# Optimization experiments

Hardware: AMD Instinct MI355X
Metric: run time of the kernel (lower is better)

The kernel has to match this reference:

```python
import jax, jax.numpy as jnp
import numpy as np

B, S, H, D_IN, DEPTH, NPHN = 128, 1024, 256, 84, 2, 40
N_HEADS = 9  # phn, word1-3, utt1-5
EPS = 1e-5


def setup_inputs() -> dict:
    key = jax.random.key(0)
    ks = jax.random.split(key, 12)
    sc = 0.02
    x = jax.random.normal(ks[0], (B, S, D_IN), jnp.float32)
    # contiguous valid prefix then -1 padding (matches get_last_valid's assumption)
    lengths = jax.random.randint(ks[1], (B,), 1, S + 1)
    phn_vals = jax.random.randint(ks[2], (B, S), 0, NPHN - 1)
    phn = jnp.where(jnp.arange(S)[None, :] < lengths[:, None], phn_vals, -1)
    return {
        "x": x,
        "phn": phn,
        "in_proj_w": jax.random.normal(ks[3], (H, D_IN), jnp.float32) * sc,
        "in_proj_b": jnp.zeros((H,), jnp.float32),
        "phn_proj_w": jax.random.normal(ks[4], (H, NPHN), jnp.float32) * sc,
        "phn_proj_b": jnp.zeros((H,), jnp.float32),
        "w_ih": jax.random.normal(ks[5], (DEPTH, 4 * H, H), jnp.float32) * sc,
        "w_hh": jax.random.normal(ks[6], (DEPTH, 4 * H, H), jnp.float32) * sc,
        "b_ih": jnp.zeros((DEPTH, 4 * H), jnp.float32),
        "b_hh": jnp.zeros((DEPTH, 4 * H), jnp.float32),
        "ln_g": jnp.ones((N_HEADS, H), jnp.float32),
        "ln_b": jnp.zeros((N_HEADS, H), jnp.float32),
        "head_w": jax.random.normal(ks[7], (N_HEADS, H), jnp.float32) * sc,
        "head_b": jnp.zeros((N_HEADS,), jnp.float32),
    }


def _lstm(h0, w_ih, w_hh, b_ih, b_hh):
    # h0: [B,S,H]; torch gate order i,f,g,o
    seq = jnp.transpose(h0, (1, 0, 2))  # [S,B,H]
    b = h0.shape[0]
    for layer in range(DEPTH):
        Wih, Whh = w_ih[layer], w_hh[layer]
        bias = b_ih[layer] + b_hh[layer]

        def step(carry, xt, Wih=Wih, Whh=Whh, bias=bias):
            hp, cp = carry
            g = xt @ Wih.T + hp @ Whh.T + bias
            i, f, gg, o = jnp.split(g, 4, axis=-1)
            c = jax.nn.sigmoid(f) * cp + jax.nn.sigmoid(i) * jnp.tanh(gg)
            hn = jax.nn.sigmoid(o) * jnp.tanh(c)
            return (hn, c), hn

        init = (jnp.zeros((b, H), h0.dtype), jnp.zeros((b, H), h0.dtype))
        _, seq = jax.lax.scan(step, init, seq)
    return jnp.transpose(seq, (1, 0, 2))  # [B,S,H]


def reference(x, phn, in_proj_w, in_proj_b, phn_proj_w, phn_proj_b,
              w_ih, w_hh, b_ih, b_hh, ln_g, ln_b, head_w, head_b):
    b, s = x.shape[0], x.shape[1]
    mask = phn >= 0  # [B,S]
    phn_oh = jax.nn.one_hot(phn + 1, NPHN, dtype=x.dtype)
    h = (x @ in_proj_w.T + in_proj_b) + (phn_oh @ phn_proj_w.T + phn_proj_b)
    hidden = _lstm(h, w_ih, w_hh, b_ih, b_hh)  # [B,S,H]

    # All 9 heads share the LN-normalized activations; fold gamma/beta into the
    # per-head linear: score_k = <xhat, gamma_k*w_k> + <beta_k, w_k> + b_k
    mu = hidden.mean(-1, keepdims=True)
    var = ((hidden - mu) ** 2).mean(-1, keepdims=True)
    xhat = (hidden - mu) * jax.lax.rsqrt(var + EPS)
    scores = (jnp.einsum('bsh,kh->bsk', xhat, ln_g * head_w)
              + (ln_b * head_w).sum(-1) + head_b)  # [B,S,9]

    # last valid token per sequence: index before first mask==0 (or S-1 if all valid)
    first_inv = jnp.argmax(~mask, axis=1)
    idx = jnp.where(mask.all(axis=1), s - 1, first_inv - 1)  # [B]
    last = scores[jnp.arange(b), idx]  # [B,9]

    p = scores[..., 0:1]
    w1, w2, w3 = scores[..., 1:2], scores[..., 2:3], scores[..., 3:4]
    u1, u2, u3, u4, u5 = (last[:, 4 + k][:, None] for k in range(5))
    return (u1, u2, u3, u4, u5, p, w1, w2, w3)
```

## Files before the change

kernel.cpp:

```cpp
#include <hip/hip_runtime.h>


typedef _Float16 h2    __attribute__((ext_vector_type(2)));
typedef _Float16 f16x8 __attribute__((ext_vector_type(8)));
typedef float    f32x4 __attribute__((ext_vector_type(4)));

#define NW_MAT 262144

static __device__ __forceinline__ float fdot2u(unsigned int w, unsigned int h, float c){
#if defined(__has_builtin) && __has_builtin(__builtin_amdgcn_fdot2)
  return __builtin_amdgcn_fdot2(__builtin_bit_cast(h2, w), __builtin_bit_cast(h2, h), c, false);
#else
  h2 a = __builtin_bit_cast(h2, w), b = __builtin_bit_cast(h2, h);
  return c + (float)a[0]*(float)b[0] + (float)a[1]*(float)b[1];
#endif
}
static __device__ __forceinline__ float sigmf(float x){ return 1.f/(1.f + __expf(-x)); }
static __device__ __forceinline__ float tanhf_(float x){ return 1.f - 2.f/(__expf(2.f*x) + 1.f); }

__global__ void k_prep(const float* __restrict__ w_ih, const float* __restrict__ w_hh,
                       const float* __restrict__ b_ih, const float* __restrict__ b_hh,
                       const float* __restrict__ ln_g, const float* __restrict__ ln_b,
                       const float* __restrict__ head_w, const float* __restrict__ head_b,
                       _Float16* wih0, _Float16* whh0, _Float16* wih1, _Float16* whh1,
                       float* bias0, float* bias1, float* vk, float* ck)
{
  int i = blockIdx.x*256 + threadIdx.x;
  if (i < NW_MAT){
    wih0[i] = (_Float16)w_ih[i];
    whh0[i] = (_Float16)w_hh[i];
    wih1[i] = (_Float16)w_ih[NW_MAT + i];
    whh1[i] = (_Float16)w_hh[NW_MAT + i];
  }
  if (i < 1024){
    bias0[i] = b_ih[i]        + b_hh[i];
    bias1[i] = b_ih[1024 + i] + b_hh[1024 + i];
  }
  if (i < 2304) vk[i] = ln_g[i]*head_w[i];
  if (i < 9){
    float s = 0.f;
    for (int h = 0; h < 256; ++h) s += ln_b[i*256 + h]*head_w[i*256 + h];
    ck[i] = s + head_b[i];
  }
}

__global__ void k_idx(const int* __restrict__ phn, int* __restrict__ idx)
{
  int b = blockIdx.x, l = threadIdx.x;
  int found = -1;
  for (int t0 = 0; t0 < 1024; t0 += 64){
    int v = phn[b*1024 + t0 + l];
    unsigned long long m = __ballot(v < 0);
    if (m){ found = t0 + (__ffsll(m) - 1); break; }
  }
  if (l == 0) idx[b] = (found < 0) ? 1023 : found - 1;
}

__global__ void k_embed(const float* __restrict__ x, const int* __restrict__ phn,
                        const float* __restrict__ ipw, const float* __restrict__ ipb,
                        const float* __restrict__ ppw, const float* __restrict__ ppb,
                        _Float16* __restrict__ E, int Tc, int LT, int tc0)
{
  __shared__ float xs[8][84];
  __shared__ int pv[8];
  int tid = threadIdx.x;
  int m0 = blockIdx.x * 8;
  for (int i = tid; i < 8*84; i += 256){
    int r = i/84, k = i - r*84;
    int m = m0 + r; int b = m >> LT; int t = tc0 + (m & (Tc-1));
    xs[r][k] = x[((size_t)b*1024 + t)*84 + k];
  }
  if (tid < 8){
    int m = m0 + tid; int b = m >> LT; int t = tc0 + (m & (Tc-1));
    pv[tid] = phn[b*1024 + t];
  }
  __syncthreads();
  float acc[8] = {0.f,0.f,0.f,0.f,0.f,0.f,0.f,0.f};
  const float* wrow = ipw + tid*84;
  for (int k = 0; k < 84; ++k){
    float wv = wrow[k];
    #pragma unroll
    for (int r = 0; r < 8; ++r) acc[r] += wv * xs[r][k];
  }
  float base = ipb[tid] + ppb[tid];
  #pragma unroll
  for (int r = 0; r < 8; ++r){
    float e = acc[r] + base + ppw[tid*40 + (pv[r] + 1)];
    E[(size_t)(m0 + r)*256 + tid] = (_Float16)e;
  }
}

__global__ __launch_bounds__(256) void k_gemm(const _Float16* __restrict__ A,
                                              const _Float16* __restrict__ Bw,
                                              const float* __restrict__ bias,
                                              _Float16* __restrict__ C)
{
  __shared__ __align__(16) _Float16 lA[128*64];
  __shared__ __align__(16) _Float16 lB[128*64];
  int tid = threadIdx.x;
  int tm = blockIdx.x, tn = blockIdx.y;
  int l = tid & 63, w = tid >> 6;
  int wm = w >> 1, wn = w & 1;
  f32x4 acc[4][4];
  #pragma unroll
  for (int mi = 0; mi < 4; ++mi)
    #pragma unroll
    for (int ni = 0; ni < 4; ++ni) acc[mi][ni] = (f32x4){0.f,0.f,0.f,0.f};
  int rr = tid >> 3, cc = tid & 7;
  #pragma unroll 1
  for (int kb = 0; kb < 4; ++kb){
    uint4 av[4], bv[4];
    #pragma unroll
    for (int i = 0; i < 4; ++i){
      int r = rr + 32*i;
      av[i] = *(const uint4*)(A  + ((size_t)(tm*128 + r))*256 + kb*64 + cc*8);
      bv[i] = *(const uint4*)(Bw + ((size_t)(tn*128 + r))*256 + kb*64 + cc*8);
    }
    __syncthreads();
    #pragma unroll
    for (int i = 0; i < 4; ++i){
      int r = rr + 32*i;
      *(uint4*)&lA[r*64 + cc*8] = av[i];
      *(uint4*)&lB[r*64 + cc*8] = bv[i];
    }
    __syncthreads();
    #pragma unroll
    for (int kk = 0; kk < 2; ++kk){
      f16x8 aF[4], bF[4];
      #pragma unroll
      for (int mi = 0; mi < 4; ++mi)
        aF[mi] = *(const f16x8*)&lA[(wm*64 + mi*16 + (l&15))*64 + kk*32 + (l>>4)*8];
      #pragma unroll
      for (int ni = 0; ni < 4; ++ni)
        bF[ni] = *(const f16x8*)&lB[(wn*64 + ni*16 + (l&15))*64 + kk*32 + (l>>4)*8];
      #pragma unroll
      for (int mi = 0; mi < 4; ++mi)
        #pragma unroll
        for (int ni = 0; ni < 4; ++ni)
          acc[mi][ni] = __builtin_amdgcn_mfma_f32_16x16x32_f16(aF[mi], bF[ni], acc[mi][ni], 0, 0, 0);
    }
  }
  #pragma unroll
  for (int mi = 0; mi < 4; ++mi){
    #pragma unroll
    for (int ni = 0; ni < 4; ++ni){
      int n = tn*128 + wn*64 + ni*16 + (l & 15);
      float bn = bias[n];
      #pragma unroll
      for (int j = 0; j < 4; ++j){
        int m = tm*128 + wm*64 + mi*16 + (l>>4)*4 + j;
        C[(size_t)m*1024 + n] = (_Float16)(acc[mi][ni][j] + bn);
      }
    }
  }
}

__global__ __launch_bounds__(512, 2) void k_lstm(const _Float16* __restrict__ G,
                                                 const _Float16* __restrict__ W,
                                                 _Float16* __restrict__ Hout,
                                                 float* __restrict__ h_state,
                                                 float* __restrict__ c_state,
                                                 int Tc, int first)
{
  __shared__ __align__(16) unsigned int h_pk_s[128];
  __shared__ float gf[1024];
  __shared__ __align__(16) unsigned int wlds[32768];
  int tid = threadIdx.x;
  int b = blockIdx.x;
  int r0 = 2*tid, r1 = r0 + 1;
  const uint4* w0s = (const uint4*)(W + (size_t)r0*256);
  const uint4* w1s = (const uint4*)(W + (size_t)r1*256);
  uint4 w0v[24], w1v[24];
  #pragma unroll
  for (int c2 = 0; c2 < 24; ++c2){ w0v[c2] = w0s[c2]; w1v[c2] = w1s[c2]; }
  #pragma unroll
  for (int c2 = 0; c2 < 24; ++c2){
    asm volatile("" : "+v"(w0v[c2].x), "+v"(w0v[c2].y), "+v"(w0v[c2].z), "+v"(w0v[c2].w),
                      "+v"(w1v[c2].x), "+v"(w1v[c2].y), "+v"(w1v[c2].z), "+v"(w1v[c2].w));
  }
  unsigned int swz = (unsigned int)(tid & 7);
  #pragma unroll
  for (int c2 = 0; c2 < 8; ++c2){
    *(uint4*)&wlds[tid*64      + (((unsigned)c2 ^ swz)*4)] = w0s[24 + c2];
    *(uint4*)&wlds[tid*64 + 32 + (((unsigned)c2 ^ swz)*4)] = w1s[24 + c2];
  }
  float c_reg = 0.f, hn = 0.f;
  if (tid < 256){
    float hv = 0.f;
    if (!first){ hv = h_state[b*256 + tid]; c_reg = c_state[b*256 + tid]; }
    ((_Float16*)h_pk_s)[tid] = (_Float16)hv;
    hn = hv;
  }
  __syncthreads();
  const unsigned int* gbase = (const unsigned int*)G + (size_t)b*Tc*512 + tid;
  _Float16* hout = Hout + (size_t)b*Tc*256;
  unsigned int gc = gbase[0];
  for (int tl = 0; tl < Tc; ++tl){
    unsigned int gn = (tl + 1 < Tc) ? gbase[(size_t)(tl + 1)*512] : 0u;
    const uint4* hp = (const uint4*)h_pk_s;
    float acc0 = 0.f, acc1 = 0.f;
    #pragma unroll
    for (int c2 = 0; c2 < 24; ++c2){
      uint4 h4 = hp[c2];
      acc0 = fdot2u(w0v[c2].x, h4.x, acc0);
      acc0 = fdot2u(w0v[c2].y, h4.y, acc0);
      acc0 = fdot2u(w0v[c2].z, h4.z, acc0);
      acc0 = fdot2u(w0v[c2].w, h4.w, acc0);
      acc1 = fdot2u(w1v[c2].x, h4.x, acc1);
      acc1 = fdot2u(w1v[c2].y, h4.y, acc1);
      acc1 = fdot2u(w1v[c2].z, h4.z, acc1);
      acc1 = fdot2u(w1v[c2].w, h4.w, acc1);
    }
    #pragma unroll
    for (int c2 = 0; c2 < 8; ++c2){
      uint4 wv0 = *(const uint4*)&wlds[tid*64      + (((unsigned)c2 ^ swz)*4)];
      uint4 wv1 = *(const uint4*)&wlds[tid*64 + 32 + (((unsigned)c2 ^ swz)*4)];
      uint4 h4 = hp[24 + c2];
      acc0 = fdot2u(wv0.x, h4.x, acc0);
      acc0 = fdot2u(wv0.y, h4.y, acc0);
      acc0 = fdot2u(wv0.z, h4.z, acc0);
      acc0 = fdot2u(wv0.w, h4.w, acc0);
      acc1 = fdot2u(wv1.x, h4.x, acc1);
      acc1 = fdot2u(wv1.y, h4.y, acc1);
      acc1 = fdot2u(wv1.z, h4.z, acc1);
      acc1 = fdot2u(wv1.w, h4.w, acc1);
    }
    h2 gp = __builtin_bit_cast(h2, gc);
    *(float2*)&gf[r0] = make_float2(acc0 + (float)gp[0], acc1 + (float)gp[1]);
    __syncthreads();
    if (tid < 256){
      float gi = gf[tid], gfr = gf[tid + 256], gg = gf[tid + 512], go = gf[tid + 768];
      float ct = sigmf(gfr)*c_reg + sigmf(gi)*tanhf_(gg);
      c_reg = ct;
      hn = sigmf(go)*tanhf_(ct);
      ((_Float16*)h_pk_s)[tid] = (_Float16)hn;
      hout[(size_t)tl*256 + tid] = (_Float16)hn;
    }
    __syncthreads();
    gc = gn;
  }
  if (tid < 256){ h_state[b*256 + tid] = hn; c_state[b*256 + tid] = c_reg; }
}

__global__ void k_ln(const _Float16* __restrict__ H1, const float* __restrict__ vk,
                     const float* __restrict__ ck, const int* __restrict__ idx,
                     float* __restrict__ out, int Tc, int LT, int tc0)
{
  __shared__ __align__(16) float vks[9*256];
  __shared__ float cks[9];
  int tid = threadIdx.x;
  for (int i = tid; i < 2304; i += 256) vks[i] = vk[i];
  if (tid < 9) cks[tid] = ck[tid];
  __syncthreads();
  int l = tid & 63, wv = tid >> 6;
  int m = blockIdx.x*4 + wv;
  int b = m >> LT; int t = tc0 + (m & (Tc-1));
  uint2 hv = *(const uint2*)(H1 + (size_t)m*256 + l*4);
  h2 pa = __builtin_bit_cast(h2, hv.x), pb = __builtin_bit_cast(h2, hv.y);
  float f0 = pa[0], f1 = pa[1], f2 = pb[0], f3 = pb[1];
  float s = f0 + f1 + f2 + f3;
  float q = f0*f0 + f1*f1 + f2*f2 + f3*f3;
  #pragma unroll
  for (int o = 32; o > 0; o >>= 1){ s += __shfl_xor(s, o, 64); q += __shfl_xor(q, o, 64); }
  float mu = s*(1.f/256.f);
  float var = q*(1.f/256.f) - mu*mu;
  float rstd = rsqrtf(var + 1e-5f);
  float xh0 = (f0 - mu)*rstd, xh1 = (f1 - mu)*rstd, xh2 = (f2 - mu)*rstd, xh3 = (f3 - mu)*rstd;
  int ib = idx[b];
  size_t rout = (size_t)b*1024 + t;
  #pragma unroll 1
  for (int k = 0; k < 9; ++k){
    float4 vvv = *(const float4*)(vks + k*256 + l*4);
    float p = xh0*vvv.x + xh1*vvv.y + xh2*vvv.z + xh3*vvv.w;
    #pragma unroll
    for (int o = 32; o > 0; o >>= 1) p += __shfl_xor(p, o, 64);
    if (l == 0){
      float sc = p + cks[k];
      if (k < 4) out[640 + (size_t)k*131072 + rout] = sc;
      else if (t == ib) out[(k - 4)*128 + b] = sc;
    }
  }
}

extern "C" void kernel_launch(void* const* d_in, const int* in_sizes, int n_in,
                              void* d_out, int out_size, void* d_ws, size_t ws_size,
                              hipStream_t stream)
{
  const float* x      = (const float*)d_in[0];
  const int*   phn    = (const int*)  d_in[1];
  const float* in_w   = (const float*)d_in[2];
  const float* in_b   = (const float*)d_in[3];
  const float* ph_w   = (const float*)d_in[4];
  const float* ph_b   = (const float*)d_in[5];
  const float* w_ih   = (const float*)d_in[6];
  const float* w_hh   = (const float*)d_in[7];
  const float* b_ih   = (const float*)d_in[8];
  const float* b_hh   = (const float*)d_in[9];
  const float* ln_g   = (const float*)d_in[10];
  const float* ln_b   = (const float*)d_in[11];
  const float* head_w = (const float*)d_in[12];
  const float* head_b = (const float*)d_in[13];
  float* out = (float*)d_out;
  char* wsb = (char*)d_ws;
  size_t o = 0;
  auto take = [&](size_t n) -> char* { char* p = wsb + o; o = (o + n + 255) & ~(size_t)255; return p; };
  _Float16* wih0 = (_Float16*)take(524288);
  _Float16* whh0 = (_Float16*)take(524288);
  _Float16* wih1 = (_Float16*)take(524288);
  _Float16* whh1 = (_Float16*)take(524288);
  float* bias0 = (float*)take(4096);
  float* bias1 = (float*)take(4096);
  float* vk    = (float*)take(9216);
  float* ck    = (float*)take(64);
  int*   idxb  = (int*)take(512);
  float* h0s = (float*)take(131072);
  float* c0s = (float*)take(131072);
  float* h1s = (float*)take(131072);
  float* c1s = (float*)take(131072);
  const size_t per_t = 3*(size_t)65536 + 1048576;
  int Tc = 1024;
  while (Tc > 8 && o + (size_t)Tc*per_t > ws_size) Tc >>= 1;
  _Float16* Eb  = (_Float16*)take((size_t)Tc*65536);
  _Float16* H0b = (_Float16*)take((size_t)Tc*65536);
  _Float16* H1b = (_Float16*)take((size_t)Tc*65536);
  _Float16* Gb  = (_Float16*)take((size_t)Tc*1048576);
  int LT = __builtin_ctz((unsigned)Tc);

  k_prep<<<1024, 256, 0, stream>>>(w_ih, w_hh, b_ih, b_hh, ln_g, ln_b, head_w, head_b,
                                   wih0, whh0, wih1, whh1, bias0, bias1, vk, ck);
  k_idx<<<128, 64, 0, stream>>>(phn, idxb);

  int M = 128*Tc;
  int nchunks = 1024/Tc;
  for (int c = 0; c < nchunks; ++c){
    int tc0 = c*Tc;
    k_embed<<<M/8, 256, 0, stream>>>(x, phn, in_w, in_b, ph_w, ph_b, Eb, Tc, LT, tc0);
    k_gemm<<<dim3(M/128, 8), 256, 0, stream>>>(Eb, wih0, bias0, Gb);
    k_lstm<<<128, 512, 0, stream>>>(Gb, whh0, H0b, h0s, c0s, Tc, c == 0 ? 1 : 0);
    k_gemm<<<dim3(M/128, 8), 256, 0, stream>>>(H0b, wih1, bias1, Gb);
    k_lstm<<<128, 512, 0, stream>>>(Gb, whh1, H1b, h1s, c1s, Tc, c == 0 ? 1 : 0);
    k_ln<<<M/4, 256, 0, stream>>>(H1b, vk, ck, idxb, out, Tc, LT, tc0);
  }
  (void)in_sizes; (void)n_in; (void)out_size;
}
```

Measured before the change: 5.637 ms.

## Add two-sequence-per-block LSTM variant and relax register pinning in layer-0 LSTM

Layer 0 now uses a variant with no asm register pins, no manual G-prefetch, an unroll-1 time loop and waves_per_eu hints. Layer 1 uses a new kernel in which each block handles two batch sequences and reads the hidden weights from global memory (L1/L2) on every step instead of keeping them in registers, so 64 blocks are launched. The goal appears to be comparing register-resident versus cache-streamed weights and halving the block count. The risk is heavy per-step global weight traffic and fewer active CUs on the serial recurrence.

```diff
diff --git a/kernel.cpp b/kernel.cpp
--- a/kernel.cpp
+++ b/kernel.cpp
@@ -155,12 +155,14 @@
   }
 }
 
-__global__ __launch_bounds__(512, 2) void k_lstm(const _Float16* __restrict__ G,
-                                                 const _Float16* __restrict__ W,
-                                                 _Float16* __restrict__ Hout,
-                                                 float* __restrict__ h_state,
-                                                 float* __restrict__ c_state,
-                                                 int Tc, int first)
+__global__ __attribute__((amdgpu_flat_work_group_size(512,512)))
+           __attribute__((amdgpu_waves_per_eu(1,2)))
+void k_lstm_v(const _Float16* __restrict__ G,
+              const _Float16* __restrict__ W,
+              _Float16* __restrict__ Hout,
+              float* __restrict__ h_state,
+              float* __restrict__ c_state,
+              int Tc, int first)
 {
   __shared__ __align__(16) unsigned int h_pk_s[128];
   __shared__ float gf[1024];
@@ -173,11 +175,6 @@
   uint4 w0v[24], w1v[24];
   #pragma unroll
   for (int c2 = 0; c2 < 24; ++c2){ w0v[c2] = w0s[c2]; w1v[c2] = w1s[c2]; }
-  #pragma unroll
-  for (int c2 = 0; c2 < 24; ++c2){
-    asm volatile("" : "+v"(w0v[c2].x), "+v"(w0v[c2].y), "+v"(w0v[c2].z), "+v"(w0v[c2].w),
-                      "+v"(w1v[c2].x), "+v"(w1v[c2].y), "+v"(w1v[c2].z), "+v"(w1v[c2].w));
-  }
   unsigned int swz = (unsigned int)(tid & 7);
   #pragma unroll
   for (int c2 = 0; c2 < 8; ++c2){
@@ -194,9 +191,9 @@
   __syncthreads();
   const unsigned int* gbase = (const unsigned int*)G + (size_t)b*Tc*512 + tid;
   _Float16* hout = Hout + (size_t)b*Tc*256;
-  unsigned int gc = gbase[0];
+  #pragma unroll 1
   for (int tl = 0; tl < Tc; ++tl){
-    unsigned int gn = (tl + 1 < Tc) ? gbase[(size_t)(tl + 1)*512] : 0u;
+    unsigned int gc = gbase[(size_t)tl*512];
     const uint4* hp = (const uint4*)h_pk_s;
     float acc0 = 0.f, acc1 = 0.f;
     #pragma unroll
@@ -237,9 +234,96 @@
       hout[(size_t)tl*256 + tid] = (_Float16)hn;
     }
     __syncthreads();
-    gc = gn;
   }
   if (tid < 256){ h_state[b*256 + tid] = hn; c_state[b*256 + tid] = c_reg; }
+}
+
+__global__ __attribute__((amdgpu_flat_work_group_size(512,512)))
+void k_lstm_c2(const _Float16* __restrict__ G,
+               const _Float16* __restrict__ W,
+               _Float16* __restrict__ Hout,
+               float* __restrict__ h_state,
+               float* __restrict__ c_state,
+               int Tc, int first)
+{
+  __shared__ __align__(16) unsigned int h_pk_s[256];
+  __shared__ float gf[2048];
+  __shared__ __align__(16) unsigned int wlds[32768];
+  int tid = threadIdx.x;
+  int b0 = blockIdx.x*2;
+  int r0 = 2*tid, r1 = r0 + 1;
+  const uint4* w0s = (const uint4*)(W + (size_t)r0*256);
+  const uint4* w1s = (const uint4*)(W + (size_t)r1*256);
+  unsigned int swz = (unsigned int)(tid & 7);
+  #pragma unroll
+  for (int c2 = 0; c2 < 8; ++c2){
+    *(uint4*)&wlds[tid*64      + (((unsigned)c2 ^ swz)*4)] = w0s[24 + c2];
+    *(uint4*)&wlds[tid*64 + 32 + (((unsigned)c2 ^ swz)*4)] = w1s[24 + c2];
+  }
+  int ch = tid >> 8, j = tid & 255;
+  float c_reg = 0.f, hn = 0.f;
+  {
+    float hv = 0.f;
+    if (!first){ hv = h_state[(b0 + ch)*256 + j]; c_reg = c_state[(b0 + ch)*256 + j]; }
+    ((_Float16*)h_pk_s)[ch*256 + j] = (_Float16)hv;
+    hn = hv;
+  }
+  __syncthreads();
+  const unsigned int* g0 = (const unsigned int*)G + (size_t)(b0    )*Tc*512 + tid;
+  const unsigned int* g1 = (const unsigned int*)G + (size_t)(b0 + 1)*Tc*512 + tid;
+  _Float16* hout = Hout + (size_t)(b0 + ch)*Tc*256 + j;
+  #pragma unroll 1
+  for (int tl = 0; tl < Tc; ++tl){
+    unsigned int gc0 = g0[(size_t)tl*512];
+    unsigned int gc1 = g1[(size_t)tl*512];
+    const uint4* hp0 = (const uint4*)h_pk_s;
+    const uint4* hp1 = hp0 + 32;
+    float a00 = 0.f, a01 = 0.f, a10 = 0.f, a11 = 0.f;
+    #pragma unroll
+    for (int c2 = 0; c2 < 24; ++c2){
+      uint4 w0 = w0s[c2], w1 = w1s[c2];
+      uint4 h40 = hp0[c2], h41 = hp1[c2];
+      a00 = fdot2u(w0.x, h40.x, a00); a00 = fdot2u(w0.y, h40.y, a00);
+      a00 = fdot2u(w0.z, h40.z, a00); a00 = fdot2u(w0.w, h40.w, a00);
+      a01 = fdot2u(w0.x, h41.x, a01); a01 = fdot2u(w0.y, h41.y, a01);
+      a01 = fdot2u(w0.z, h41.z, a01); a01 = fdot2u(w0.w, h41.w, a01);
+      a10 = fdot2u(w1.x, h40.x, a10); a10 = fdot2u(w1.y, h40.y, a10);
+      a10 = fdot2u(w1.z, h40.z, a10); a10 = fdot2u(w1.w, h40.w, a10);
+      a11 = fdot2u(w1.x, h41.x, a11); a11 = fdot2u(w1.y, h41.y, a11);
+      a11 = fdot2u(w1.z, h41.z, a11); a11 = fdot2u(w1.w, h41.w, a11);
+    }
+    #pragma unroll
+    for (int c2 = 0; c2 < 8; ++c2){
+      uint4 w0 = *(const uint4*)&wlds[tid*64      + (((unsigned)c2 ^ swz)*4)];
+      uint4 w1 = *(const uint4*)&wlds[tid*64 + 32 + (((unsigned)c2 ^ swz)*4)];
+      uint4 h40 = hp0[24 + c2], h41 = hp1[24 + c2];
+      a00 = fdot2u(w0.x, h40.x, a00); a00 = fdot2u(w0.y, h40.y, a00);
+      a00 = fdot2u(w0.z, h40.z, a00); a00 = fdot2u(w0.w, h40.w, a00);
+      a01 = fdot2u(w0.x, h41.x, a01); a01 = fdot2u(w0.y, h41.y, a01);
+      a01 = fdot2u(w0.z, h41.z, a01); a01 = fdot2u(w0.w, h41.w, a01);
+      a10 = fdot2u(w1.x, h40.x, a10); a10 = fdot2u(w1.y, h40.y, a10);
+      a10 = fdot2u(w1.z, h40.z, a10); a10 = fdot2u(w1.w, h40.w, a10);
+      a11 = fdot2u(w1.x, h41.x, a11); a11 = fdot2u(w1.y, h41.y, a11);
+      a11 = fdot2u(w1.z, h41.z, a11); a11 = fdot2u(w1.w, h41.w, a11);
+    }
+    h2 gp0 = __builtin_bit_cast(h2, gc0);
+    h2 gp1 = __builtin_bit_cast(h2, gc1);
+    *(float2*)&gf[r0]        = make_float2(a00 + (float)gp0[0], a10 + (float)gp0[1]);
+    *(float2*)&gf[1024 + r0] = make_float2(a01 + (float)gp1[0], a11 + (float)gp1[1]);
+    __syncthreads();
+    {
+      float gi  = gf[ch*1024 + j],       gfr = gf[ch*1024 + j + 256];
+      float gg  = gf[ch*1024 + j + 512], go  = gf[ch*1024 + j + 768];
+      float ct = sigmf(gfr)*c_reg + sigmf(gi)*tanhf_(gg);
+      c_reg = ct;
+      hn = sigmf(go)*tanhf_(ct);
+      ((_Float16*)h_pk_s)[ch*256 + j] = (_Float16)hn;
+      hout[(size_t)tl*256] = (_Float16)hn;
+    }
+    __syncthreads();
+  }
+  h_state[(b0 + ch)*256 + j] = hn;
+  c_state[(b0 + ch)*256 + j] = c_reg;
 }
 
 __global__ void k_ln(const _Float16* __restrict__ H1, const float* __restrict__ vk,
@@ -336,9 +420,9 @@
     int tc0 = c*Tc;
     k_embed<<<M/8, 256, 0, stream>>>(x, phn, in_w, in_b, ph_w, ph_b, Eb, Tc, LT, tc0);
     k_gemm<<<dim3(M/128, 8), 256, 0, stream>>>(Eb, wih0, bias0, Gb);
-    k_lstm<<<128, 512, 0, stream>>>(Gb, whh0, H0b, h0s, c0s, Tc, c == 0 ? 1 : 0);
+    k_lstm_v<<<128, 512, 0, stream>>>(Gb, whh0, H0b, h0s, c0s, Tc, c == 0 ? 1 : 0);
     k_gemm<<<dim3(M/128, 8), 256, 0, stream>>>(H0b, wih1, bias1, Gb);
-    k_lstm<<<128, 512, 0, stream>>>(Gb, whh1, H1b, h1s, c1s, Tc, c == 0 ? 1 : 0);
+    k_lstm_c2<<<64, 512, 0, stream>>>(Gb, whh1, H1b, h1s, c1s, Tc, c == 0 ? 1 : 0);
     k_ln<<<M/4, 256, 0, stream>>>(H1b, vk, ck, idxb, out, Tc, LT, tc0);
   }
   (void)in_sizes; (void)n_in; (void)out_size;
```

Result: slower. 7.258 ms (+28.7%).
